# Performance work log

Hardware: AMD Instinct MI355X
Metric: run time of the kernel (lower is better)

Reference implementation:

```python
import jax, jax.numpy as jnp
import numpy as np

B, C, HH, WW = 16, 512, 32, 32
NUM_HEADS = 8
NUM_GROUPS = 32
EPS = 1e-5


def setup_inputs() -> dict:
    key = jax.random.key(0)
    ks = jax.random.split(key, 4)
    x = jax.random.normal(ks[0], (B, C, HH, WW), dtype=jnp.float32)
    gn_scale = jnp.ones((C,), dtype=jnp.float32)
    gn_bias = jnp.zeros((C,), dtype=jnp.float32)
    qkv_w = jax.random.normal(ks[1], (3 * C, C), dtype=jnp.float32) * (1.0 / np.sqrt(C))
    qkv_b = jnp.zeros((3 * C,), dtype=jnp.float32)
    # NOTE: original zero-inits proj_out; we use random weights for a non-trivial baseline.
    proj_w = jax.random.normal(ks[2], (C, C), dtype=jnp.float32) * (1.0 / np.sqrt(C))
    proj_b = jnp.zeros((C,), dtype=jnp.float32)
    return {"x": x, "gn_scale": gn_scale, "gn_bias": gn_bias,
            "qkv_w": qkv_w, "qkv_b": qkv_b, "proj_w": proj_w, "proj_b": proj_b}


def reference(x, gn_scale, gn_bias, qkv_w, qkv_b, proj_w, proj_b):
    b, c, h, w = x.shape
    t = h * w
    nh = NUM_HEADS
    d = c // nh
    xf = x.reshape(b, c, t)                      # (B, C, T)

    # GroupNorm(32, C) over (channels-in-group, spatial)
    xg = xf.reshape(b, NUM_GROUPS, (c // NUM_GROUPS) * t)
    mu = jnp.mean(xg, axis=-1, keepdims=True)
    var = jnp.var(xg, axis=-1, keepdims=True)
    xn = ((xg - mu) * jax.lax.rsqrt(var + EPS)).reshape(b, c, t)
    xn = xn * gn_scale[:, None] + gn_bias[:, None]

    # 1x1 conv QKV: (3C, C) matmul over channel dim
    qkv = jnp.einsum('oc,bct->bot', qkv_w, xn) + qkv_b[:, None]
    # channel axis splits as (3, H, D) per rearrange 'B (three H C) T -> three B T H C'
    qkv = qkv.reshape(b, 3, nh, d, t)
    q, k, v = qkv[:, 0], qkv[:, 1], qkv[:, 2]    # each (B, H, D, T)

    scale = 1.0 / jnp.sqrt(jnp.asarray(d, x.dtype))
    logits = jnp.einsum('bhdt,bhds->bhts', q, k) * scale   # (B, H, T, S)
    probs = jax.nn.softmax(logits, axis=-1)
    attn = jnp.einsum('bhts,bhds->bhdt', probs, v)         # (B, H, D, T)

    hout = attn.reshape(b, c, t)                 # 'B T H C -> B (H C) T'
    hout = jnp.einsum('oc,bct->bot', proj_w, hout) + proj_b[:, None]
    return (hout + xf).reshape(b, c, h, w)
```

## Files before the change

### kernel.cpp

```cpp
#include <hip/hip_runtime.h>

typedef unsigned short ushort_t;
typedef unsigned int uint_t;
typedef __bf16 bf16x8 __attribute__((ext_vector_type(8)));
typedef float f32x4 __attribute__((ext_vector_type(4)));
typedef uint_t u32x4 __attribute__((ext_vector_type(4)));
typedef uint_t u32x2 __attribute__((ext_vector_type(2)));


static __device__ __forceinline__ ushort_t f2bf(float f) {
  union { float f; uint_t u; } v; v.f = f;
  uint_t r = v.u + 0x7FFFu + ((v.u >> 16) & 1u);
  return (ushort_t)(r >> 16);
}

static __device__ __forceinline__ uint_t cvt_pk_bf16(float lo, float hi) {
  uint_t r;
  asm("v_cvt_pk_bf16_f32 %0, %1, %2" : "=v"(r) : "v"(lo), "v"(hi));
  return r;
}

static __device__ __forceinline__ f32x4 mfma_bf16(bf16x8 a, bf16x8 b, f32x4 c) {
  return __builtin_amdgcn_mfma_f32_16x16x32_bf16(a, b, c, 0, 0, 0);
}

__global__ __launch_bounds__(256) void k_convert(const float* __restrict__ src,
                                                 ushort_t* __restrict__ dst, int n) {
  int i = (blockIdx.x * 256 + threadIdx.x) * 4;
  if (i >= n) return;
  f32x4 v = *(const f32x4*)(src + i);
  u32x2 o;
  o[0] = (uint_t)f2bf(v[0]) | ((uint_t)f2bf(v[1]) << 16);
  o[1] = (uint_t)f2bf(v[2]) | ((uint_t)f2bf(v[3]) << 16);
  *(u32x2*)(dst + i) = o;
}

__global__ __launch_bounds__(256) void k_gn(const float* __restrict__ x,
                                            const float* __restrict__ gsc,
                                            const float* __restrict__ gbi,
                                            ushort_t* __restrict__ xnT) {
  const int g = blockIdx.x, b = blockIdx.y;
  const int tid = threadIdx.x;
  const float* xp = x + ((size_t)b * 512 + g * 16) * 1024;

  float s = 0.f, q = 0.f;
#pragma unroll
  for (int i = 0; i < 16; ++i) {
    f32x4 v = *(const f32x4*)(xp + (tid + i * 256) * 4);
    s += v[0] + v[1] + v[2] + v[3];
    q += v[0]*v[0] + v[1]*v[1] + v[2]*v[2] + v[3]*v[3];
  }
#pragma unroll
  for (int off = 32; off > 0; off >>= 1) { s += __shfl_xor(s, off); q += __shfl_xor(q, off); }

  __shared__ float rs[4], rq[4], ssc[16], sbi[16], stats[2];
  if ((tid & 63) == 0) { rs[tid >> 6] = s; rq[tid >> 6] = q; }
  if (tid < 16) { ssc[tid] = gsc[g * 16 + tid]; sbi[tid] = gbi[g * 16 + tid]; }
  __syncthreads();
  if (tid == 0) {
    float S = rs[0] + rs[1] + rs[2] + rs[3];
    float Q = rq[0] + rq[1] + rq[2] + rq[3];
    float mean = S * (1.f / 16384.f);
    float var  = Q * (1.f / 16384.f) - mean * mean;
    stats[0] = mean; stats[1] = rsqrtf(var + 1e-5f);
  }
  __syncthreads();
  const float mean = stats[0], rstd = stats[1];

#pragma unroll
  for (int i = 0; i < 8; ++i) {
    int u = tid + i * 256;
    int t = u >> 1, half = u & 1;
    union { ushort_t us[8]; u32x4 v4; } o;
#pragma unroll
    for (int j = 0; j < 8; ++j) {
      int c = half * 8 + j;
      float v = (xp[(size_t)c * 1024 + t] - mean) * rstd * ssc[c] + sbi[c];
      o.us[j] = f2bf(v);
    }
    *(u32x4*)(xnT + ((size_t)b * 1024 + t) * 512 + g * 16 + half * 8) = o.v4;
  }
}

__global__ __launch_bounds__(256) void k_qkv(const ushort_t* __restrict__ xnT,
                                             const ushort_t* __restrict__ Wbf,
                                             const float* __restrict__ bias,
                                             ushort_t* __restrict__ qkT,
                                             ushort_t* __restrict__ vbuf) {
  const int mi = blockIdx.x, ni = blockIdx.y, b = blockIdx.z;
  const int tid = threadIdx.x, lane = tid & 63, w = tid >> 6;
  const int wm = w >> 1, wn = w & 1;
  const int lr = lane & 15, lg = lane >> 4;

  __shared__ __align__(16) ushort_t As[128 * 40];
  __shared__ __align__(16) ushort_t Bs[128 * 40];
  __shared__ __align__(16) float tbuf[32 * 132];

  const ushort_t* Ap = xnT + (size_t)b * 1024 * 512 + (size_t)mi * 128 * 512;
  const ushort_t* Bp = Wbf + (size_t)ni * 128 * 512;

  const int row0 = tid >> 2, seg = tid & 3;
  u32x4 ra0, ra1, rb0, rb1;

  ra0 = *(const u32x4*)(Ap + (size_t)row0 * 512 + seg * 8);
  ra1 = *(const u32x4*)(Ap + (size_t)(row0 + 64) * 512 + seg * 8);
  rb0 = *(const u32x4*)(Bp + (size_t)row0 * 512 + seg * 8);
  rb1 = *(const u32x4*)(Bp + (size_t)(row0 + 64) * 512 + seg * 8);
  *(u32x4*)(As + row0 * 40 + seg * 8) = ra0;
  *(u32x4*)(As + (row0 + 64) * 40 + seg * 8) = ra1;
  *(u32x4*)(Bs + row0 * 40 + seg * 8) = rb0;
  *(u32x4*)(Bs + (row0 + 64) * 40 + seg * 8) = rb1;
  __syncthreads();

  f32x4 acc[4][4] = {};

  for (int kt = 0; kt < 16; ++kt) {
    if (kt < 15) {
      const int k0n = (kt + 1) * 32;
      ra0 = *(const u32x4*)(Ap + (size_t)row0 * 512 + k0n + seg * 8);
      ra1 = *(const u32x4*)(Ap + (size_t)(row0 + 64) * 512 + k0n + seg * 8);
      rb0 = *(const u32x4*)(Bp + (size_t)row0 * 512 + k0n + seg * 8);
      rb1 = *(const u32x4*)(Bp + (size_t)(row0 + 64) * 512 + k0n + seg * 8);
    }
    bf16x8 af[4], bfv[4];
#pragma unroll
    for (int i = 0; i < 4; ++i)
      af[i] = *(const bf16x8*)(As + (wm * 64 + i * 16 + lr) * 40 + lg * 8);
#pragma unroll
    for (int j = 0; j < 4; ++j)
      bfv[j] = *(const bf16x8*)(Bs + (wn * 64 + j * 16 + lr) * 40 + lg * 8);
    __builtin_amdgcn_s_setprio(1);
#pragma unroll
    for (int i = 0; i < 4; ++i)
#pragma unroll
      for (int j = 0; j < 4; ++j)
        acc[i][j] = mfma_bf16(af[i], bfv[j], acc[i][j]);
    __builtin_amdgcn_s_setprio(0);
    if (kt < 15) {
      __syncthreads();
      *(u32x4*)(As + row0 * 40 + seg * 8) = ra0;
      *(u32x4*)(As + (row0 + 64) * 40 + seg * 8) = ra1;
      *(u32x4*)(Bs + row0 * 40 + seg * 8) = rb0;
      *(u32x4*)(Bs + (row0 + 64) * 40 + seg * 8) = rb1;
      __syncthreads();
    }
  }

  float biasv[4];
#pragma unroll
  for (int j = 0; j < 4; ++j) biasv[j] = bias[ni * 128 + wn * 64 + j * 16 + lr];

  if (ni < 8) {
    const float oscale = (ni >= 4) ? 0.1803368801f : 1.0f;
    ushort_t* outp = qkT + ((size_t)b * 1024 + mi * 128) * 1024 + ni * 128;
#pragma unroll
    for (int i = 0; i < 4; ++i)
#pragma unroll
      for (int j = 0; j < 4; ++j)
#pragma unroll
        for (int r = 0; r < 4; ++r) {
          const int m = wm * 64 + i * 16 + lg * 4 + r;
          const int n = wn * 64 + j * 16 + lr;
          outp[(size_t)m * 1024 + n] = f2bf((acc[i][j][r] + biasv[j]) * oscale);
        }
  } else {
    ushort_t* tb = (ushort_t*)tbuf;
#pragma unroll
    for (int c = 0; c < 4; ++c) {
      if (wn == (c >> 1)) {
#pragma unroll
        for (int jj = 0; jj < 2; ++jj) {
          const int j = (c & 1) * 2 + jj;
#pragma unroll
          for (int i = 0; i < 4; ++i)
#pragma unroll
            for (int r = 0; r < 4; ++r) {
              const int m = wm * 64 + i * 16 + lg * 4 + r;
              const int nl = jj * 16 + lr;
              tb[nl * 136 + m] = f2bf(acc[i][j][r] + biasv[j]);
            }
        }
      }
      __syncthreads();
      for (int u = tid; u < 512; u += 256) {
        const int nl = u >> 4, sg = u & 15;
        const int op = ni * 128 + c * 32 + nl - 1024;
        *(u32x4*)(vbuf + ((size_t)b * 512 + op) * 1024 + mi * 128 + sg * 8) =
            *(const u32x4*)(tb + nl * 136 + sg * 8);
      }
      __syncthreads();
    }
  }
}

#define PSTR 68
__global__ __launch_bounds__(256) void k_attn(const ushort_t* __restrict__ qkT,
                                              const ushort_t* __restrict__ vbuf,
                                              ushort_t* __restrict__ attnT) {
  const int bid = blockIdx.x;
  const int xcd = bid & 7;
  const int qt  = (bid >> 3) & 7;
  const int hb  = ((bid >> 6) << 3) | xcd;
  const int h   = hb & 7, b = hb >> 3;
  const int tid = threadIdx.x, lane = tid & 63, w = tid >> 6;
  const int lr = lane & 15, lg = lane >> 4;

  __shared__ __align__(16) ushort_t Ks[64 * PSTR];
  __shared__ __align__(16) ushort_t Vs[64 * PSTR];
  __shared__ __align__(16) ushort_t Ps[4 * 32 * PSTR];

  bf16x8 aq[2][2];
#pragma unroll
  for (int tI = 0; tI < 2; ++tI) {
    const int t = qt * 128 + w * 32 + tI * 16 + lr;
    const ushort_t* qp = qkT + ((size_t)b * 1024 + t) * 1024 + h * 64 + lg * 8;
    aq[tI][0] = *(const bf16x8*)(qp);
    aq[tI][1] = *(const bf16x8*)(qp + 32);
  }

  f32x4 oacc[2][4] = {};
  float lrun[2] = {0.f, 0.f};

  const size_t vbase = ((size_t)b * 512 + h * 64) * 1024;
  const size_t kbase = (size_t)b * 1024 * 1024 + 512 + h * 64;
  ushort_t* Pw = Ps + w * 32 * PSTR;

  const int srow = tid >> 3, sseg = tid & 7;
  u32x4 kr0, kr1, vr0, vr1;

  kr0 = *(const u32x4*)(qkT + kbase + (size_t)srow * 1024 + sseg * 8);
  kr1 = *(const u32x4*)(qkT + kbase + (size_t)(srow + 32) * 1024 + sseg * 8);
  vr0 = *(const u32x4*)(vbuf + vbase + (size_t)srow * 1024 + sseg * 8);
  vr1 = *(const u32x4*)(vbuf + vbase + (size_t)(srow + 32) * 1024 + sseg * 8);
  *(u32x4*)(Ks + srow * PSTR + sseg * 8) = kr0;
  *(u32x4*)(Ks + (srow + 32) * PSTR + sseg * 8) = kr1;
  *(u32x4*)(Vs + srow * PSTR + sseg * 8) = vr0;
  *(u32x4*)(Vs + (srow + 32) * PSTR + sseg * 8) = vr1;
  __syncthreads();

  for (int st = 0; st < 16; ++st) {
    if (st < 15) {
      const int s0n = (st + 1) * 64;
      kr0 = *(const u32x4*)(qkT + kbase + (size_t)(s0n + srow) * 1024 + sseg * 8);
      kr1 = *(const u32x4*)(qkT + kbase + (size_t)(s0n + srow + 32) * 1024 + sseg * 8);
      vr0 = *(const u32x4*)(vbuf + vbase + (size_t)srow * 1024 + s0n + sseg * 8);
      vr1 = *(const u32x4*)(vbuf + vbase + (size_t)(srow + 32) * 1024 + s0n + sseg * 8);
    }

    f32x4 sacc[2][4] = {};
    __builtin_amdgcn_s_setprio(1);
#pragma unroll
    for (int sI = 0; sI < 4; ++sI) {
      const bf16x8 bk0 = *(const bf16x8*)(Ks + (sI * 16 + lr) * PSTR + lg * 8);
      const bf16x8 bk1 = *(const bf16x8*)(Ks + (sI * 16 + lr) * PSTR + 32 + lg * 8);
#pragma unroll
      for (int tI = 0; tI < 2; ++tI) {
        sacc[tI][sI] = mfma_bf16(bk0, aq[tI][0], sacc[tI][sI]);
        sacc[tI][sI] = mfma_bf16(bk1, aq[tI][1], sacc[tI][sI]);
      }
    }
    __builtin_amdgcn_s_setprio(0);

#pragma unroll
    for (int tI = 0; tI < 2; ++tI)
#pragma unroll
      for (int sI = 0; sI < 4; ++sI)
#pragma unroll
        for (int r = 0; r < 4; ++r)
          sacc[tI][sI][r] = __builtin_amdgcn_exp2f(sacc[tI][sI][r]);
#pragma unroll
    for (int tI = 0; tI < 2; ++tI) {
      float a0 = (sacc[tI][0][0] + sacc[tI][0][1]) + (sacc[tI][0][2] + sacc[tI][0][3]);
      float a1 = (sacc[tI][1][0] + sacc[tI][1][1]) + (sacc[tI][1][2] + sacc[tI][1][3]);
      float a2 = (sacc[tI][2][0] + sacc[tI][2][1]) + (sacc[tI][2][2] + sacc[tI][2][3]);
      float a3 = (sacc[tI][3][0] + sacc[tI][3][1]) + (sacc[tI][3][2] + sacc[tI][3][3]);
      lrun[tI] += (a0 + a1) + (a2 + a3);
    }

#pragma unroll
    for (int tI = 0; tI < 2; ++tI)
#pragma unroll
      for (int sI = 0; sI < 4; ++sI) {
        u32x2 d;
        d[0] = cvt_pk_bf16(sacc[tI][sI][0], sacc[tI][sI][1]);
        d[1] = cvt_pk_bf16(sacc[tI][sI][2], sacc[tI][sI][3]);
        *(u32x2*)(Pw + (tI * 16 + lr) * PSTR + sI * 16 + lg * 4) = d;
      }

#pragma unroll
    for (int tI = 0; tI < 2; ++tI) {
      const bf16x8 ap0 = *(const bf16x8*)(Pw + (tI * 16 + lr) * PSTR + lg * 8);
      const bf16x8 ap1 = *(const bf16x8*)(Pw + (tI * 16 + lr) * PSTR + 32 + lg * 8);
      __builtin_amdgcn_s_setprio(1);
#pragma unroll
      for (int dI = 0; dI < 4; ++dI) {
        const bf16x8 bv0 = *(const bf16x8*)(Vs + (dI * 16 + lr) * PSTR + lg * 8);
        const bf16x8 bv1 = *(const bf16x8*)(Vs + (dI * 16 + lr) * PSTR + 32 + lg * 8);
        oacc[tI][dI] = mfma_bf16(ap0, bv0, oacc[tI][dI]);
        oacc[tI][dI] = mfma_bf16(ap1, bv1, oacc[tI][dI]);
      }
      __builtin_amdgcn_s_setprio(0);
    }

    if (st < 15) {
      __syncthreads();
      *(u32x4*)(Ks + srow * PSTR + sseg * 8) = kr0;
      *(u32x4*)(Ks + (srow + 32) * PSTR + sseg * 8) = kr1;
      *(u32x4*)(Vs + srow * PSTR + sseg * 8) = vr0;
      *(u32x4*)(Vs + (srow + 32) * PSTR + sseg * 8) = vr1;
      __syncthreads();
    }
  }

  float inv[2][4];
#pragma unroll
  for (int tI = 0; tI < 2; ++tI) {
    float tot = lrun[tI];
    tot += __shfl_xor(tot, 16);
    tot += __shfl_xor(tot, 32);
#pragma unroll
    for (int r = 0; r < 4; ++r) {
      inv[tI][r] = 1.f / __shfl(tot, (lane & 48) | (lg * 4 + r));
    }
  }
#pragma unroll
  for (int tI = 0; tI < 2; ++tI)
#pragma unroll
    for (int dI = 0; dI < 4; ++dI)
#pragma unroll
      for (int r = 0; r < 4; ++r) {
        const int t = qt * 128 + w * 32 + tI * 16 + lg * 4 + r;
        attnT[((size_t)b * 1024 + t) * 512 + h * 64 + dI * 16 + lr] =
            f2bf(oacc[tI][dI][r] * inv[tI][r]);
      }
}

__global__ __launch_bounds__(256) void k_proj(const ushort_t* __restrict__ attnT,
                                              const ushort_t* __restrict__ Wbf,
                                              const float* __restrict__ bias,
                                              const float* __restrict__ xres,
                                              float* __restrict__ outp) {
  const int mi = blockIdx.x, ni = blockIdx.y, b = blockIdx.z;
  const int tid = threadIdx.x, lane = tid & 63, w = tid >> 6;
  const int wm = w >> 1, wn = w & 1;
  const int lr = lane & 15, lg = lane >> 4;

  __shared__ __align__(16) ushort_t As[128 * 40];
  __shared__ __align__(16) ushort_t Bs[128 * 40];
  __shared__ __align__(16) float tbuf[32 * 132];

  const ushort_t* Ap = attnT + (size_t)b * 1024 * 512 + (size_t)mi * 128 * 512;
  const ushort_t* Bp = Wbf + (size_t)ni * 128 * 512;

  const int row0 = tid >> 2, seg = tid & 3;
  u32x4 ra0, ra1, rb0, rb1;

  ra0 = *(const u32x4*)(Ap + (size_t)row0 * 512 + seg * 8);
  ra1 = *(const u32x4*)(Ap + (size_t)(row0 + 64) * 512 + seg * 8);
  rb0 = *(const u32x4*)(Bp + (size_t)row0 * 512 + seg * 8);
  rb1 = *(const u32x4*)(Bp + (size_t)(row0 + 64) * 512 + seg * 8);
  *(u32x4*)(As + row0 * 40 + seg * 8) = ra0;
  *(u32x4*)(As + (row0 + 64) * 40 + seg * 8) = ra1;
  *(u32x4*)(Bs + row0 * 40 + seg * 8) = rb0;
  *(u32x4*)(Bs + (row0 + 64) * 40 + seg * 8) = rb1;
  __syncthreads();

  f32x4 acc[4][4] = {};

  for (int kt = 0; kt < 16; ++kt) {
    if (kt < 15) {
      const int k0n = (kt + 1) * 32;
      ra0 = *(const u32x4*)(Ap + (size_t)row0 * 512 + k0n + seg * 8);
      ra1 = *(const u32x4*)(Ap + (size_t)(row0 + 64) * 512 + k0n + seg * 8);
      rb0 = *(const u32x4*)(Bp + (size_t)row0 * 512 + k0n + seg * 8);
      rb1 = *(const u32x4*)(Bp + (size_t)(row0 + 64) * 512 + k0n + seg * 8);
    }
    bf16x8 af[4], bfv[4];
#pragma unroll
    for (int i = 0; i < 4; ++i)
      af[i] = *(const bf16x8*)(As + (wm * 64 + i * 16 + lr) * 40 + lg * 8);
#pragma unroll
    for (int j = 0; j < 4; ++j)
      bfv[j] = *(const bf16x8*)(Bs + (wn * 64 + j * 16 + lr) * 40 + lg * 8);
    __builtin_amdgcn_s_setprio(1);
#pragma unroll
    for (int i = 0; i < 4; ++i)
#pragma unroll
      for (int j = 0; j < 4; ++j)
        acc[i][j] = mfma_bf16(af[i], bfv[j], acc[i][j]);
    __builtin_amdgcn_s_setprio(0);
    if (kt < 15) {
      __syncthreads();
      *(u32x4*)(As + row0 * 40 + seg * 8) = ra0;
      *(u32x4*)(As + (row0 + 64) * 40 + seg * 8) = ra1;
      *(u32x4*)(Bs + row0 * 40 + seg * 8) = rb0;
      *(u32x4*)(Bs + (row0 + 64) * 40 + seg * 8) = rb1;
      __syncthreads();
    }
  }

  float biasv[4];
#pragma unroll
  for (int j = 0; j < 4; ++j) biasv[j] = bias[ni * 128 + wn * 64 + j * 16 + lr];

#pragma unroll
  for (int c = 0; c < 4; ++c) {
    if (wn == (c >> 1)) {
#pragma unroll
      for (int jj = 0; jj < 2; ++jj) {
        const int j = (c & 1) * 2 + jj;
#pragma unroll
        for (int i = 0; i < 4; ++i)
#pragma unroll
          for (int r = 0; r < 4; ++r) {
            const int m = wm * 64 + i * 16 + lg * 4 + r;
            const int nl = jj * 16 + lr;
            tbuf[nl * 132 + m] = acc[i][j][r] + biasv[j];
          }
      }
    }
    __syncthreads();
    for (int u = tid; u < 1024; u += 256) {
      const int nl = u >> 5, sg = u & 31;
      const int o = ni * 128 + c * 32 + nl;
      const size_t idx = ((size_t)b * 512 + o) * 1024 + mi * 128 + sg * 4;
      const f32x4 t = *(const f32x4*)(tbuf + nl * 132 + sg * 4);
      const f32x4 xr = *(const f32x4*)(xres + idx);
      f32x4 ov = t + xr;
      *(f32x4*)(outp + idx) = ov;
    }
    __syncthreads();
  }
}

extern "C" void kernel_launch(void* const* d_in, const int* in_sizes, int n_in,
                              void* d_out, int out_size, void* d_ws, size_t ws_size,
                              hipStream_t stream) {
  (void)in_sizes; (void)n_in; (void)out_size; (void)ws_size;
  const float* x      = (const float*)d_in[0];
  const float* gsc    = (const float*)d_in[1];
  const float* gbi    = (const float*)d_in[2];
  const float* qkv_w  = (const float*)d_in[3];
  const float* qkv_b  = (const float*)d_in[4];
  const float* proj_w = (const float*)d_in[5];
  const float* proj_b = (const float*)d_in[6];
  float* out = (float*)d_out;

  char* ws = (char*)d_ws;
  ushort_t* xnT   = (ushort_t*)(ws);
  ushort_t* qkT   = (ushort_t*)(ws + 16777216);
  ushort_t* vbuf  = (ushort_t*)(ws + 50331648);
  ushort_t* attnT = (ushort_t*)(ws + 67108864);
  ushort_t* qwbf  = (ushort_t*)(ws + 83886080);
  ushort_t* pwbf  = (ushort_t*)(ws + 85458944);

  k_convert<<<768, 256, 0, stream>>>(qkv_w, qwbf, 1536 * 512);
  k_convert<<<256, 256, 0, stream>>>(proj_w, pwbf, 512 * 512);
  k_gn<<<dim3(32, 16), 256, 0, stream>>>(x, gsc, gbi, xnT);
  k_qkv<<<dim3(8, 12, 16), 256, 0, stream>>>(xnT, qwbf, qkv_b, qkT, vbuf);
  k_attn<<<1024, 256, 0, stream>>>(qkT, vbuf, attnT);
  k_proj<<<dim3(8, 4, 16), 256, 0, stream>>>(attnT, pwbf, proj_b, x, out);
}
```

Measured before the change: 238.7 us.

## Use direct global-to-LDS loads with double-buffered tiles in QKV and projection GEMMs

Replaces the register-staged global loads and LDS stores in the QKV and output-projection GEMM main loops with global_load_lds 16-byte transfers straight into shared memory. The A/B tiles become double-buffered and unpadded (stride 32), so each k-step needs one barrier instead of two. This aims to cut VGPR staging and LDS write instructions and to overlap the next tile's fetch with MFMA work. The unpadded stride may add LDS bank conflicts, and correctness relies on the per-wave lane layout of global_load_lds matching the row indexing used for reads.

```diff
diff --git a/kernel.cpp b/kernel.cpp
--- a/kernel.cpp
+++ b/kernel.cpp
@@ -22,6 +22,12 @@
 
 static __device__ __forceinline__ f32x4 mfma_bf16(bf16x8 a, bf16x8 b, f32x4 c) {
   return __builtin_amdgcn_mfma_f32_16x16x32_bf16(a, b, c, 0, 0, 0);
+}
+
+static __device__ __forceinline__ void gload16(const ushort_t* g, ushort_t* l) {
+  __builtin_amdgcn_global_load_lds(
+      (const __attribute__((address_space(1))) uint_t*)g,
+      (__attribute__((address_space(3))) uint_t*)l, 16, 0, 0);
 }
 
 __global__ __launch_bounds__(256) void k_convert(const float* __restrict__ src,
@@ -92,43 +98,41 @@
   const int wm = w >> 1, wn = w & 1;
   const int lr = lane & 15, lg = lane >> 4;
 
-  __shared__ __align__(16) ushort_t As[128 * 40];
-  __shared__ __align__(16) ushort_t Bs[128 * 40];
+  __shared__ __align__(16) ushort_t As[2][4096];
+  __shared__ __align__(16) ushort_t Bs[2][4096];
   __shared__ __align__(16) float tbuf[32 * 132];
 
   const ushort_t* Ap = xnT + (size_t)b * 1024 * 512 + (size_t)mi * 128 * 512;
   const ushort_t* Bp = Wbf + (size_t)ni * 128 * 512;
 
-  const int row0 = tid >> 2, seg = tid & 3;
-  u32x4 ra0, ra1, rb0, rb1;
-
-  ra0 = *(const u32x4*)(Ap + (size_t)row0 * 512 + seg * 8);
-  ra1 = *(const u32x4*)(Ap + (size_t)(row0 + 64) * 512 + seg * 8);
-  rb0 = *(const u32x4*)(Bp + (size_t)row0 * 512 + seg * 8);
-  rb1 = *(const u32x4*)(Bp + (size_t)(row0 + 64) * 512 + seg * 8);
-  *(u32x4*)(As + row0 * 40 + seg * 8) = ra0;
-  *(u32x4*)(As + (row0 + 64) * 40 + seg * 8) = ra1;
-  *(u32x4*)(Bs + row0 * 40 + seg * 8) = rb0;
-  *(u32x4*)(Bs + (row0 + 64) * 40 + seg * 8) = rb1;
+  const int r0 = tid >> 2, sg = tid & 3;
+  const int wbase0 = w * 512;
+  const int wbase1 = 2048 + w * 512;
+
+  gload16(Ap + (size_t)r0 * 512 + sg * 8,        &As[0][wbase0]);
+  gload16(Ap + (size_t)(r0 + 64) * 512 + sg * 8, &As[0][wbase1]);
+  gload16(Bp + (size_t)r0 * 512 + sg * 8,        &Bs[0][wbase0]);
+  gload16(Bp + (size_t)(r0 + 64) * 512 + sg * 8, &Bs[0][wbase1]);
   __syncthreads();
 
   f32x4 acc[4][4] = {};
 
   for (int kt = 0; kt < 16; ++kt) {
+    const int cur = kt & 1;
     if (kt < 15) {
       const int k0n = (kt + 1) * 32;
-      ra0 = *(const u32x4*)(Ap + (size_t)row0 * 512 + k0n + seg * 8);
-      ra1 = *(const u32x4*)(Ap + (size_t)(row0 + 64) * 512 + k0n + seg * 8);
-      rb0 = *(const u32x4*)(Bp + (size_t)row0 * 512 + k0n + seg * 8);
-      rb1 = *(const u32x4*)(Bp + (size_t)(row0 + 64) * 512 + k0n + seg * 8);
+      gload16(Ap + (size_t)r0 * 512 + k0n + sg * 8,        &As[cur ^ 1][wbase0]);
+      gload16(Ap + (size_t)(r0 + 64) * 512 + k0n + sg * 8, &As[cur ^ 1][wbase1]);
+      gload16(Bp + (size_t)r0 * 512 + k0n + sg * 8,        &Bs[cur ^ 1][wbase0]);
+      gload16(Bp + (size_t)(r0 + 64) * 512 + k0n + sg * 8, &Bs[cur ^ 1][wbase1]);
     }
     bf16x8 af[4], bfv[4];
 #pragma unroll
     for (int i = 0; i < 4; ++i)
-      af[i] = *(const bf16x8*)(As + (wm * 64 + i * 16 + lr) * 40 + lg * 8);
+      af[i] = *(const bf16x8*)(&As[cur][(wm * 64 + i * 16 + lr) * 32 + lg * 8]);
 #pragma unroll
     for (int j = 0; j < 4; ++j)
-      bfv[j] = *(const bf16x8*)(Bs + (wn * 64 + j * 16 + lr) * 40 + lg * 8);
+      bfv[j] = *(const bf16x8*)(&Bs[cur][(wn * 64 + j * 16 + lr) * 32 + lg * 8]);
     __builtin_amdgcn_s_setprio(1);
 #pragma unroll
     for (int i = 0; i < 4; ++i)
@@ -136,14 +140,7 @@
       for (int j = 0; j < 4; ++j)
         acc[i][j] = mfma_bf16(af[i], bfv[j], acc[i][j]);
     __builtin_amdgcn_s_setprio(0);
-    if (kt < 15) {
-      __syncthreads();
-      *(u32x4*)(As + row0 * 40 + seg * 8) = ra0;
-      *(u32x4*)(As + (row0 + 64) * 40 + seg * 8) = ra1;
-      *(u32x4*)(Bs + row0 * 40 + seg * 8) = rb0;
-      *(u32x4*)(Bs + (row0 + 64) * 40 + seg * 8) = rb1;
-      __syncthreads();
-    }
+    __syncthreads();
   }
 
   float biasv[4];
@@ -183,10 +180,10 @@
       }
       __syncthreads();
       for (int u = tid; u < 512; u += 256) {
-        const int nl = u >> 4, sg = u & 15;
+        const int nl = u >> 4, sgx = u & 15;
         const int op = ni * 128 + c * 32 + nl - 1024;
-        *(u32x4*)(vbuf + ((size_t)b * 512 + op) * 1024 + mi * 128 + sg * 8) =
-            *(const u32x4*)(tb + nl * 136 + sg * 8);
+        *(u32x4*)(vbuf + ((size_t)b * 512 + op) * 1024 + mi * 128 + sgx * 8) =
+            *(const u32x4*)(tb + nl * 136 + sgx * 8);
       }
       __syncthreads();
     }
@@ -319,9 +316,8 @@
     tot += __shfl_xor(tot, 16);
     tot += __shfl_xor(tot, 32);
 #pragma unroll
-    for (int r = 0; r < 4; ++r) {
+    for (int r = 0; r < 4; ++r)
       inv[tI][r] = 1.f / __shfl(tot, (lane & 48) | (lg * 4 + r));
-    }
   }
 #pragma unroll
   for (int tI = 0; tI < 2; ++tI)
@@ -345,43 +341,41 @@
   const int wm = w >> 1, wn = w & 1;
   const int lr = lane & 15, lg = lane >> 4;
 
-  __shared__ __align__(16) ushort_t As[128 * 40];
-  __shared__ __align__(16) ushort_t Bs[128 * 40];
+  __shared__ __align__(16) ushort_t As[2][4096];
+  __shared__ __align__(16) ushort_t Bs[2][4096];
   __shared__ __align__(16) float tbuf[32 * 132];
 
   const ushort_t* Ap = attnT + (size_t)b * 1024 * 512 + (size_t)mi * 128 * 512;
   const ushort_t* Bp = Wbf + (size_t)ni * 128 * 512;
 
-  const int row0 = tid >> 2, seg = tid & 3;
-  u32x4 ra0, ra1, rb0, rb1;
-
-  ra0 = *(const u32x4*)(Ap + (size_t)row0 * 512 + seg * 8);
-  ra1 = *(const u32x4*)(Ap + (size_t)(row0 + 64) * 512 + seg * 8);
-  rb0 = *(const u32x4*)(Bp + (size_t)row0 * 512 + seg * 8);
-  rb1 = *(const u32x4*)(Bp + (size_t)(row0 + 64) * 512 + seg * 8);
-  *(u32x4*)(As + row0 * 40 + seg * 8) = ra0;
-  *(u32x4*)(As + (row0 + 64) * 40 + seg * 8) = ra1;
-  *(u32x4*)(Bs + row0 * 40 + seg * 8) = rb0;
-  *(u32x4*)(Bs + (row0 + 64) * 40 + seg * 8) = rb1;
+  const int r0 = tid >> 2, sg = tid & 3;
+  const int wbase0 = w * 512;
+  const int wbase1 = 2048 + w * 512;
+
+  gload16(Ap + (size_t)r0 * 512 + sg * 8,        &As[0][wbase0]);
+  gload16(Ap + (size_t)(r0 + 64) * 512 + sg * 8, &As[0][wbase1]);
+  gload16(Bp + (size_t)r0 * 512 + sg * 8,        &Bs[0][wbase0]);
+  gload16(Bp + (size_t)(r0 + 64) * 512 + sg * 8, &Bs[0][wbase1]);
   __syncthreads();
 
   f32x4 acc[4][4] = {};
 
   for (int kt = 0; kt < 16; ++kt) {
+    const int cur = kt & 1;
     if (kt < 15) {
       const int k0n = (kt + 1) * 32;
-      ra0 = *(const u32x4*)(Ap + (size_t)row0 * 512 + k0n + seg * 8);
-      ra1 = *(const u32x4*)(Ap + (size_t)(row0 + 64) * 512 + k0n + seg * 8);
-      rb0 = *(const u32x4*)(Bp + (size_t)row0 * 512 + k0n + seg * 8);
-      rb1 = *(const u32x4*)(Bp + (size_t)(row0 + 64) * 512 + k0n + seg * 8);
+      gload16(Ap + (size_t)r0 * 512 + k0n + sg * 8,        &As[cur ^ 1][wbase0]);
+      gload16(Ap + (size_t)(r0 + 64) * 512 + k0n + sg * 8, &As[cur ^ 1][wbase1]);
+      gload16(Bp + (size_t)r0 * 512 + k0n + sg * 8,        &Bs[cur ^ 1][wbase0]);
+      gload16(Bp + (size_t)(r0 + 64) * 512 + k0n + sg * 8, &Bs[cur ^ 1][wbase1]);
     }
     bf16x8 af[4], bfv[4];
 #pragma unroll
     for (int i = 0; i < 4; ++i)
-      af[i] = *(const bf16x8*)(As + (wm * 64 + i * 16 + lr) * 40 + lg * 8);
+      af[i] = *(const bf16x8*)(&As[cur][(wm * 64 + i * 16 + lr) * 32 + lg * 8]);
 #pragma unroll
     for (int j = 0; j < 4; ++j)
-      bfv[j] = *(const bf16x8*)(Bs + (wn * 64 + j * 16 + lr) * 40 + lg * 8);
+      bfv[j] = *(const bf16x8*)(&Bs[cur][(wn * 64 + j * 16 + lr) * 32 + lg * 8]);
     __builtin_amdgcn_s_setprio(1);
 #pragma unroll
     for (int i = 0; i < 4; ++i)
@@ -389,14 +383,7 @@
       for (int j = 0; j < 4; ++j)
         acc[i][j] = mfma_bf16(af[i], bfv[j], acc[i][j]);
     __builtin_amdgcn_s_setprio(0);
-    if (kt < 15) {
-      __syncthreads();
-      *(u32x4*)(As + row0 * 40 + seg * 8) = ra0;
-      *(u32x4*)(As + (row0 + 64) * 40 + seg * 8) = ra1;
-      *(u32x4*)(Bs + row0 * 40 + seg * 8) = rb0;
-      *(u32x4*)(Bs + (row0 + 64) * 40 + seg * 8) = rb1;
-      __syncthreads();
-    }
+    __syncthreads();
   }
 
   float biasv[4];
@@ -421,10 +408,10 @@
     }
     __syncthreads();
     for (int u = tid; u < 1024; u += 256) {
-      const int nl = u >> 5, sg = u & 31;
+      const int nl = u >> 5, sgx = u & 31;
       const int o = ni * 128 + c * 32 + nl;
-      const size_t idx = ((size_t)b * 512 + o) * 1024 + mi * 128 + sg * 4;
-      const f32x4 t = *(const f32x4*)(tbuf + nl * 132 + sg * 4);
+      const size_t idx = ((size_t)b * 512 + o) * 1024 + mi * 128 + sgx * 4;
+      const f32x4 t = *(const f32x4*)(tbuf + nl * 132 + sgx * 4);
       const f32x4 xr = *(const f32x4*)(xres + idx);
       f32x4 ov = t + xr;
       *(f32x4*)(outp + idx) = ov;
```

Measured after the change: 234.6 us. No clear change (-1.7%).
